# Kernel tuning notes

Measured on AMD Instinct MI355X. Metric: run time of the kernel, lower is better.

## Reference

```python
import jax, jax.numpy as jnp
import numpy as np
from jax import lax

C = 96          # channels (d_model)
D_STATE = 16
D_CONV = 4
EXPAND = 2
D_INNER = EXPAND * C          # 192
DT_RANK = (C + 15) // 16      # 6 (ceil(d_model/16), mamba_ssm default)
B, H, W = 4, 96, 96
LN_EPS = 1e-5


def setup_inputs() -> dict:
    key = jax.random.key(0)
    ks = jax.random.split(key, 10)
    s = 0.02
    return {
        "spatial_feat": jax.random.normal(ks[0], (B, C, H, W), jnp.float32),
        "freq_feat":    jax.random.normal(ks[1], (B, C, H, W), jnp.float32),
        # fusion proj: nn.Linear(2C, C) with bias
        "proj_w": jax.random.normal(ks[2], (C, 2 * C), jnp.float32) * s,
        "proj_b": jnp.zeros((C,), jnp.float32),
        # Mamba params (mamba_ssm defaults: in/x/out proj bias=False, conv bias=True)
        "in_proj_w": jax.random.normal(ks[3], (2 * D_INNER, C), jnp.float32) * s,
        "conv_w": jax.random.normal(ks[4], (D_INNER, 1, D_CONV), jnp.float32) * s,
        "conv_b": jnp.zeros((D_INNER,), jnp.float32),
        "x_proj_w": jax.random.normal(ks[5], (DT_RANK + 2 * D_STATE, D_INNER), jnp.float32) * s,
        "dt_proj_w": jax.random.normal(ks[6], (D_INNER, DT_RANK), jnp.float32) * s,
        "dt_proj_b": jnp.full((D_INNER,), -4.6, jnp.float32),  # softplus ~ 0.01
        "A_log": jnp.log(jnp.tile(jnp.arange(1, D_STATE + 1, dtype=jnp.float32), (D_INNER, 1))),
        "D_param": jnp.ones((D_INNER,), jnp.float32),
        "out_proj_w": jax.random.normal(ks[7], (C, D_INNER), jnp.float32) * s,
        "ln_g": jnp.ones((C,), jnp.float32),
        "ln_b": jnp.zeros((C,), jnp.float32),
    }


def _mamba_fusion(spatial_feat, freq_feat, proj_w, proj_b, in_proj_w, conv_w,
                  conv_b, x_proj_w, dt_proj_w, dt_proj_b, A_log, D_param,
                  out_proj_w, ln_g, ln_b):
    Bsz, Ch, Hh, Ww = spatial_feat.shape
    L = Hh * Ww
    # concat + flatten(2).transpose(1,2): [B, L, 2C]
    seq = jnp.concatenate([spatial_feat, freq_feat], axis=1).reshape(Bsz, 2 * Ch, L).transpose(0, 2, 1)
    x = seq @ proj_w.T + proj_b  # [B, L, C]

    # ---- Mamba mixer ----
    xz = x @ in_proj_w.T                      # [B, L, 2*d_inner]
    x_in, z = jnp.split(xz, 2, axis=-1)
    # causal depthwise conv1d over sequence
    xc = lax.conv_general_dilated(
        x_in.transpose(0, 2, 1), conv_w, (1,), [(D_CONV - 1, 0)],
        dimension_numbers=('NCH', 'OIH', 'NCH'), feature_group_count=D_INNER)
    xc = jax.nn.silu(xc + conv_b[None, :, None]).transpose(0, 2, 1)  # [B, L, d_inner]

    x_dbl = xc @ x_proj_w.T                   # [B, L, dt_rank + 2*d_state]
    dt, Bm, Cm = jnp.split(x_dbl, [DT_RANK, DT_RANK + D_STATE], axis=-1)
    delta = jax.nn.softplus(dt @ dt_proj_w.T + dt_proj_b)  # [B, L, d_inner]
    A = -jnp.exp(A_log)                       # [d_inner, d_state]

    def step(h, inp):
        d_t, B_t, C_t, x_t = inp              # [B,d_in],[B,ds],[B,ds],[B,d_in]
        h = jnp.exp(d_t[:, :, None] * A) * h + (d_t * x_t)[:, :, None] * B_t[:, None, :]
        y_t = jnp.einsum('bds,bs->bd', h, C_t)
        return h, y_t

    xs = (delta.transpose(1, 0, 2), Bm.transpose(1, 0, 2),
          Cm.transpose(1, 0, 2), xc.transpose(1, 0, 2))
    h0 = jnp.zeros((Bsz, D_INNER, D_STATE), x.dtype)
    _, ys = lax.scan(step, h0, xs)            # ys: [L, B, d_inner]
    y = ys.transpose(1, 0, 2) + xc * D_param
    y = y * jax.nn.silu(z)
    mixed = y @ out_proj_w.T                  # [B, L, C]

    # LayerNorm over channel dim
    mu = mixed.mean(-1, keepdims=True)
    var = mixed.var(-1, keepdims=True)
    normed = (mixed - mu) * lax.rsqrt(var + LN_EPS) * ln_g + ln_b

    fused = normed.transpose(0, 2, 1).reshape(Bsz, Ch, Hh, Ww)
    return fused + spatial_feat


def reference(spatial_feat, freq_feat, proj_w, proj_b, in_proj_w, conv_w,
              conv_b, x_proj_w, dt_proj_w, dt_proj_b, A_log, D_param,
              out_proj_w, ln_g, ln_b):
    return _mamba_fusion(spatial_feat, freq_feat, proj_w, proj_b, in_proj_w,
                         conv_w, conv_b, x_proj_w, dt_proj_w, dt_proj_b,
                         A_log, D_param, out_proj_w, ln_g, ln_b)
```

## Files before the change

kernel.cpp:

```cpp
#include <hip/hip_runtime.h>
#include <math.h>

#define kC    96
#define kL    9216
#define kB    4
#define kDI   192
#define kDS   16
#define kDTR  6
#define kCL   128
#define kNC   72
#define kNROW (kB*kL)
#define kNSEQ (kB*kDI*kDS)

__device__ __forceinline__ float silu_f(float v) { return v / (1.f + expf(-v)); }

__global__ __launch_bounds__(256)
void k0_prep(const float* __restrict__ proj_w, const float* __restrict__ proj_b,
             const float* __restrict__ in_proj_w, const float* __restrict__ A_log,
             float* __restrict__ WcT, float* __restrict__ bias_c, float* __restrict__ A)
{
    int idx = blockIdx.x * 256 + threadIdx.x;
    if (idx < 384 * 192) {
        int co = idx / 192;
        int k  = idx % 192;
        float acc = 0.f;
        #pragma unroll 4
        for (int c = 0; c < 96; ++c)
            acc += in_proj_w[co * 96 + c] * proj_w[c * 192 + k];
        WcT[k * 384 + co] = acc;
    }
    if (idx < 384) {
        float acc = 0.f;
        for (int c = 0; c < 96; ++c) acc += in_proj_w[idx * 96 + c] * proj_b[c];
        bias_c[idx] = acc;
    }
    if (idx < kDI * kDS) {
        A[idx] = -expf(A_log[idx]);
    }
}

__global__ __launch_bounds__(256)
void k1_xz(const float* __restrict__ spatial, const float* __restrict__ freq,
           const float* __restrict__ WcT, const float* __restrict__ bias_c,
           float* __restrict__ x_in, float* __restrict__ z)
{
    __shared__ float As[192 * 36];
    const int t   = threadIdx.x;
    const int blk = blockIdx.x;
    const int b   = blk / 288;
    const int l0  = (blk % 288) * 32;

    #pragma unroll
    for (int i = 0; i < 6; ++i) {
        int e  = i * 256 + t;
        int k  = e >> 3, lg = e & 7;
        const float* src = (k < 96)
            ? &spatial[(size_t)(b * 96 + k) * kL]
            : &freq   [(size_t)(b * 96 + (k - 96)) * kL];
        float4 v = *(const float4*)&src[l0 + lg * 4];
        *(float4*)&As[k * 36 + lg * 4] = v;
    }
    __syncthreads();

    const int w    = t >> 6;
    const int lane = t & 63;
    float acc[6][8];
    #pragma unroll
    for (int i = 0; i < 6; ++i) {
        float bc = bias_c[lane + 64 * i];
        #pragma unroll
        for (int l = 0; l < 8; ++l) acc[i][l] = bc;
    }

    const float* wp = WcT + lane;
    #pragma unroll 2
    for (int k = 0; k < 192; ++k) {
        const float4 a0 = *(const float4*)&As[k * 36 + w * 8];
        const float4 a1 = *(const float4*)&As[k * 36 + w * 8 + 4];
        float wv[6];
        #pragma unroll
        for (int i = 0; i < 6; ++i) wv[i] = wp[k * 384 + 64 * i];
        #pragma unroll
        for (int i = 0; i < 6; ++i) {
            acc[i][0] += wv[i] * a0.x;  acc[i][1] += wv[i] * a0.y;
            acc[i][2] += wv[i] * a0.z;  acc[i][3] += wv[i] * a0.w;
            acc[i][4] += wv[i] * a1.x;  acc[i][5] += wv[i] * a1.y;
            acc[i][6] += wv[i] * a1.z;  acc[i][7] += wv[i] * a1.w;
        }
    }

    const size_t rbase = (size_t)b * kL + l0 + w * 8;
    #pragma unroll
    for (int l = 0; l < 8; ++l) {
        const size_t ro = (rbase + l) * 192;
        #pragma unroll
        for (int i = 0; i < 3; ++i)
            x_in[ro + lane + 64 * i] = acc[i][l];
        #pragma unroll
        for (int i = 3; i < 6; ++i)
            z[ro + lane + 64 * i - 192] = acc[i][l];
    }
}

__global__ __launch_bounds__(256)
void k2_conv(const float* __restrict__ x_in, const float* __restrict__ conv_w,
             const float* __restrict__ conv_b, float* __restrict__ xc)
{
    int idx = blockIdx.x * 256 + threadIdx.x;
    if (idx >= kNROW * 48) return;
    const int d4 = idx % 48;
    const int r  = idx / 48;
    const int l  = r % kL;
    const int d0 = d4 * 4;
    float ax = 0.f, ay = 0.f, az = 0.f, aw = 0.f;
    #pragma unroll
    for (int k = 0; k < 4; ++k) {
        int li = l - 3 + k;
        if (li < 0) continue;
        const float4 xv = *(const float4*)&x_in[(size_t)(r - 3 + k) * 192 + d0];
        ax += xv.x * conv_w[(d0 + 0) * 4 + k];
        ay += xv.y * conv_w[(d0 + 1) * 4 + k];
        az += xv.z * conv_w[(d0 + 2) * 4 + k];
        aw += xv.w * conv_w[(d0 + 3) * 4 + k];
    }
    float4 o;
    o.x = silu_f(ax + conv_b[d0 + 0]);
    o.y = silu_f(ay + conv_b[d0 + 1]);
    o.z = silu_f(az + conv_b[d0 + 2]);
    o.w = silu_f(aw + conv_b[d0 + 3]);
    *(float4*)&xc[(size_t)r * 192 + d0] = o;
}

__global__ __launch_bounds__(256)
void k34(const float* __restrict__ xc, const float* __restrict__ x_proj_w,
         const float* __restrict__ dt_proj_w, const float* __restrict__ dt_proj_b,
         float* __restrict__ BC, float* __restrict__ delta)
{
    __shared__ float xcT[192 * 65];
    __shared__ float bc_s[64 * 33];
    __shared__ float dtr_s[64 * 9];
    const int t = threadIdx.x;
    const size_t R0 = (size_t)blockIdx.x * 64;

    #pragma unroll
    for (int i = 0; i < 12; ++i) {
        int e = i * 256 + t;
        int r = e / 48, k4 = e % 48;
        float4 v = *(const float4*)&xc[(R0 + r) * 192 + k4 * 4];
        xcT[(k4 * 4 + 0) * 65 + r] = v.x;
        xcT[(k4 * 4 + 1) * 65 + r] = v.y;
        xcT[(k4 * 4 + 2) * 65 + r] = v.z;
        xcT[(k4 * 4 + 3) * 65 + r] = v.w;
    }
    __syncthreads();

    const int lane = t & 63;
    const int w = __builtin_amdgcn_readfirstlane(t >> 6);

    float acc[10];
    #pragma unroll
    for (int i = 0; i < 10; ++i) acc[i] = 0.f;
    int jj[10];
    #pragma unroll
    for (int i = 0; i < 10; ++i) { int j = w + 4 * i; jj[i] = (j < 38) ? j : 37; }

    #pragma unroll 4
    for (int k = 0; k < 192; ++k) {
        const float xv = xcT[k * 65 + lane];
        #pragma unroll
        for (int i = 0; i < 10; ++i)
            acc[i] += xv * x_proj_w[jj[i] * 192 + k];
    }

    #pragma unroll
    for (int i = 0; i < 10; ++i) {
        int j = w + 4 * i;
        if (j < 6)       dtr_s[lane * 9 + j] = acc[i];
        else if (j < 38) bc_s[lane * 33 + (j - 6)] = acc[i];
    }
    __syncthreads();

    #pragma unroll
    for (int i = 0; i < 2; ++i) {
        int e = i * 256 + t;
        int r = e >> 3, j4 = e & 7;
        float4 v;
        v.x = bc_s[r * 33 + j4 * 4 + 0];
        v.y = bc_s[r * 33 + j4 * 4 + 1];
        v.z = bc_s[r * 33 + j4 * 4 + 2];
        v.w = bc_s[r * 33 + j4 * 4 + 3];
        *(float4*)&BC[(R0 + r) * 32 + j4 * 4] = v;
    }

    {
        float dtv[6];
        #pragma unroll
        for (int j = 0; j < 6; ++j) dtv[j] = dtr_s[lane * 9 + j];
        #pragma unroll 4
        for (int m = 0; m < 48; ++m) {
            const int d = w * 48 + m;
            float a = dt_proj_b[d];
            #pragma unroll
            for (int j = 0; j < 6; ++j) a += dtv[j] * dt_proj_w[d * 6 + j];
            float sp = (a > 20.f) ? a : log1pf(expf(a));
            xcT[d * 65 + lane] = sp;
        }
    }
    __syncthreads();

    #pragma unroll
    for (int i = 0; i < 12; ++i) {
        int e = i * 256 + t;
        int r = e / 48, d4 = e % 48;
        float4 v;
        v.x = xcT[(d4 * 4 + 0) * 65 + r];
        v.y = xcT[(d4 * 4 + 1) * 65 + r];
        v.z = xcT[(d4 * 4 + 2) * 65 + r];
        v.w = xcT[(d4 * 4 + 3) * 65 + r];
        *(float4*)&delta[(R0 + r) * 192 + d4 * 4] = v;
    }
}

__global__ __launch_bounds__(256)
void k5_scan1(const float* __restrict__ delta, const float* __restrict__ xc,
              const float* __restrict__ BC, const float* __restrict__ A,
              float* __restrict__ Pc, float* __restrict__ Sc)
{
    const int wid  = (blockIdx.x * 256 + threadIdx.x) >> 6;
    const int lane = threadIdx.x & 63;
    const int c  = wid % kNC;
    const int dg = (wid / kNC) % 48;
    const int b  = wid / (kNC * 48);
    const int s  = lane & 15;
    const int d  = dg * 4 + (lane >> 4);
    const float Ads = A[dg * 64 + lane];

    const size_t rbase = (size_t)b * kL + (size_t)c * kCL;
    const float* dp = delta + rbase * 192 + d;
    const float* xp = xc    + rbase * 192 + d;
    const float* bp = BC    + rbase * 32  + s;

    float P = 1.f, S = 0.f;
    #pragma unroll 4
    for (int i = 0; i < kCL; ++i) {
        float dv = *dp, xv = *xp, bv = *bp;
        float a  = __expf(dv * Ads);
        float bt = dv * xv * bv;
        P *= a;
        S  = a * S + bt;
        dp += 192; xp += 192; bp += 32;
    }
    const int row = (b * 192 + d) * 16 + s;
    Pc[(size_t)c * kNSEQ + row] = P;
    Sc[(size_t)c * kNSEQ + row] = S;
}

__global__ __launch_bounds__(256)
void k6_cscan(const float* __restrict__ Pc, const float* __restrict__ Sc,
              float* __restrict__ hin)
{
    const int row = blockIdx.x * 256 + threadIdx.x;
    float h = 0.f;
    for (int c = 0; c < kNC; ++c) {
        size_t o = (size_t)c * kNSEQ + row;
        hin[o] = h;
        h = Pc[o] * h + Sc[o];
    }
}

__global__ __launch_bounds__(256)
void k7_scan2(const float* __restrict__ delta, const float* __restrict__ xc,
              const float* __restrict__ BC, const float* __restrict__ A,
              const float* __restrict__ hin, float* __restrict__ ys)
{
    const int wid  = (blockIdx.x * 256 + threadIdx.x) >> 6;
    const int lane = threadIdx.x & 63;
    const int c  = wid % kNC;
    const int dg = (wid / kNC) % 48;
    const int b  = wid / (kNC * 48);
    const int s  = lane & 15;
    const int d  = dg * 4 + (lane >> 4);
    const float Ads = A[dg * 64 + lane];
    const int row = (b * 192 + d) * 16 + s;

    const size_t rbase = (size_t)b * kL + (size_t)c * kCL;
    const float* dp = delta + rbase * 192 + d;
    const float* xp = xc    + rbase * 192 + d;
    const float* bp = BC    + rbase * 32  + s;
    const float* cp = BC    + rbase * 32  + 16 + s;
    float*       yp = ys    + rbase * 192 + d;

    float h = hin[(size_t)c * kNSEQ + row];
    for (int i = 0; i < kCL; ++i) {
        float dv = *dp, xv = *xp, bv = *bp, cv = *cp;
        float a = __expf(dv * Ads);
        h = a * h + dv * xv * bv;
        float pv = h * cv;
        pv += __shfl_xor(pv, 1);
        pv += __shfl_xor(pv, 2);
        pv += __shfl_xor(pv, 4);
        pv += __shfl_xor(pv, 8);
        if (s == 0) *yp = pv;
        dp += 192; xp += 192; bp += 32; cp += 32; yp += 192;
    }
}

__global__ __launch_bounds__(256)
void k8_final(const float* __restrict__ ys, const float* __restrict__ xc,
              const float* __restrict__ z, const float* __restrict__ Dp,
              const float* __restrict__ out_proj_w, const float* __restrict__ ln_g,
              const float* __restrict__ ln_b, const float* __restrict__ spatial,
              float* __restrict__ out)
{
    __shared__ float yt[32 * 196];
    __shared__ float wt[96 * 36];
    const int t = threadIdx.x;
    const size_t r0 = (size_t)blockIdx.x * 32;
    const int b = (int)(r0 / kL);

    #pragma unroll
    for (int i = 0; i < 6; ++i) {
        int e  = i * 256 + t;
        int l  = e / 48, d4 = e % 48;
        size_t r = r0 + l;
        float4 yv = *(const float4*)&ys[r * 192 + d4 * 4];
        float4 xv = *(const float4*)&xc[r * 192 + d4 * 4];
        float4 zv = *(const float4*)&z [r * 192 + d4 * 4];
        float4 Dv = *(const float4*)&Dp[d4 * 4];
        float4 o;
        o.x = (yv.x + xv.x * Dv.x) * silu_f(zv.x);
        o.y = (yv.y + xv.y * Dv.y) * silu_f(zv.y);
        o.z = (yv.z + xv.z * Dv.z) * silu_f(zv.z);
        o.w = (yv.w + xv.w * Dv.w) * silu_f(zv.w);
        *(float4*)&yt[l * 196 + d4 * 4] = o;
    }
    __syncthreads();

    const int l  = t >> 3;
    const int cg = t & 7;
    float acc[12];
    #pragma unroll
    for (int i = 0; i < 12; ++i) acc[i] = 0.f;

    for (int kc = 0; kc < 6; ++kc) {
        __syncthreads();
        #pragma unroll
        for (int i = 0; i < 3; ++i) {
            int e = i * 256 + t;
            int c = e / 8, k4 = e % 8;
            float4 w = *(const float4*)&out_proj_w[c * 192 + kc * 32 + k4 * 4];
            *(float4*)&wt[c * 36 + k4 * 4] = w;
        }
        __syncthreads();
        #pragma unroll
        for (int k4 = 0; k4 < 8; ++k4) {
            float4 yv = *(const float4*)&yt[l * 196 + kc * 32 + k4 * 4];
            #pragma unroll
            for (int i = 0; i < 12; ++i) {
                const float4 wv = *(const float4*)&wt[(cg + 8 * i) * 36 + k4 * 4];
                acc[i] += yv.x * wv.x + yv.y * wv.y + yv.z * wv.z + yv.w * wv.w;
            }
        }
    }

    float sum = 0.f, ss = 0.f;
    #pragma unroll
    for (int i = 0; i < 12; ++i) { sum += acc[i]; ss += acc[i] * acc[i]; }
    #pragma unroll
    for (int m = 1; m < 8; m <<= 1) {
        sum += __shfl_xor(sum, m);
        ss  += __shfl_xor(ss, m);
    }
    const float mu  = sum * (1.f / 96.f);
    const float var = ss * (1.f / 96.f) - mu * mu;
    const float rs  = rsqrtf(var + 1e-5f);
    const int lg = (int)(r0 % kL) + l;
    #pragma unroll
    for (int i = 0; i < 12; ++i) {
        int c = cg + 8 * i;
        float nv = (acc[i] - mu) * rs * ln_g[c] + ln_b[c];
        size_t o = ((size_t)b * 96 + c) * kL + lg;
        out[o] = nv + spatial[o];
    }
}

extern "C" void kernel_launch(void* const* d_in, const int* in_sizes, int n_in,
                              void* d_out, int out_size, void* d_ws, size_t ws_size,
                              hipStream_t stream) {
    const float* spatial    = (const float*)d_in[0];
    const float* freq       = (const float*)d_in[1];
    const float* proj_w     = (const float*)d_in[2];
    const float* proj_b     = (const float*)d_in[3];
    const float* in_proj_w  = (const float*)d_in[4];
    const float* conv_w     = (const float*)d_in[5];
    const float* conv_b     = (const float*)d_in[6];
    const float* x_proj_w   = (const float*)d_in[7];
    const float* dt_proj_w  = (const float*)d_in[8];
    const float* dt_proj_b  = (const float*)d_in[9];
    const float* A_log      = (const float*)d_in[10];
    const float* D_param    = (const float*)d_in[11];
    const float* out_proj_w = (const float*)d_in[12];
    const float* ln_g       = (const float*)d_in[13];
    const float* ln_b       = (const float*)d_in[14];
    float* out = (float*)d_out;

    char* wsb = (char*)d_ws;
    size_t off = 0;
    auto alloc = [&](size_t bytes) -> float* {
        float* p = (float*)(wsb + off);
        off += (bytes + 255) & ~(size_t)255;
        return p;
    };
    float* x_in  = alloc((size_t)kNROW * kDI * 4);
    float* z     = alloc((size_t)kNROW * kDI * 4);
    float* xc    = alloc((size_t)kNROW * kDI * 4);
    float* delta = alloc((size_t)kNROW * kDI * 4);
    float* BC    = alloc((size_t)kNROW * 32 * 4);
    float* Pc    = alloc((size_t)kNC * kNSEQ * 4);
    float* Sc    = alloc((size_t)kNC * kNSEQ * 4);
    float* hin   = alloc((size_t)kNC * kNSEQ * 4);
    float* WcT   = alloc((size_t)192 * 384 * 4);
    float* biasc = alloc(384 * 4);
    float* Aa    = alloc((size_t)kDI * kDS * 4);
    float* ys    = x_in;

    k0_prep <<<288,  256, 0, stream>>>(proj_w, proj_b, in_proj_w, A_log, WcT, biasc, Aa);
    k1_xz   <<<1152, 256, 0, stream>>>(spatial, freq, WcT, biasc, x_in, z);
    k2_conv <<<6912, 256, 0, stream>>>(x_in, conv_w, conv_b, xc);
    k34     <<<576,  256, 0, stream>>>(xc, x_proj_w, dt_proj_w, dt_proj_b, BC, delta);
    k5_scan1<<<3456, 256, 0, stream>>>(delta, xc, BC, Aa, Pc, Sc);
    k6_cscan<<<48,   256, 0, stream>>>(Pc, Sc, hin);
    k7_scan2<<<3456, 256, 0, stream>>>(delta, xc, BC, Aa, hin, ys);
    k8_final<<<1152, 256, 0, stream>>>(ys, xc, z, D_param, out_proj_w, ln_g, ln_b, spatial, out);
}
```

Before: 557.3 us.

## Transpose scan inputs to time-major per channel and precompute delta*x

k34 now writes delta, delta*x and the B/C projections in a channel-major, sequence-contiguous layout. This lets both scan kernels read float4 vectors along time instead of doing strided 192-float loads. The scan2 kernel prefetches the next float4 group and writes its y output in the same transposed layout. k8_final transposes y back through shared memory, which adds LDS work and extra shared memory per block. The transposed stores from k34 are scalar stores that are only partly coalesced.

Result: slower. 608.3 us (+9.1%).

```diff
diff --git a/kernel.cpp b/kernel.cpp
--- a/kernel.cpp
+++ b/kernel.cpp
@@ -134,13 +134,15 @@
 __global__ __launch_bounds__(256)
 void k34(const float* __restrict__ xc, const float* __restrict__ x_proj_w,
          const float* __restrict__ dt_proj_w, const float* __restrict__ dt_proj_b,
-         float* __restrict__ BC, float* __restrict__ delta)
+         float* __restrict__ BCt, float* __restrict__ dT, float* __restrict__ duT)
 {
     __shared__ float xcT[192 * 65];
     __shared__ float bc_s[64 * 33];
     __shared__ float dtr_s[64 * 9];
     const int t = threadIdx.x;
     const size_t R0 = (size_t)blockIdx.x * 64;
+    const int b  = (int)(R0 / kL);
+    const int l0 = (int)(R0 % kL);
 
     #pragma unroll
     for (int i = 0; i < 12; ++i) {
@@ -181,49 +183,30 @@
     __syncthreads();
 
     #pragma unroll
-    for (int i = 0; i < 2; ++i) {
+    for (int i = 0; i < 8; ++i) {
         int e = i * 256 + t;
-        int r = e >> 3, j4 = e & 7;
-        float4 v;
-        v.x = bc_s[r * 33 + j4 * 4 + 0];
-        v.y = bc_s[r * 33 + j4 * 4 + 1];
-        v.z = bc_s[r * 33 + j4 * 4 + 2];
-        v.w = bc_s[r * 33 + j4 * 4 + 3];
-        *(float4*)&BC[(R0 + r) * 32 + j4 * 4] = v;
-    }
-
-    {
-        float dtv[6];
-        #pragma unroll
-        for (int j = 0; j < 6; ++j) dtv[j] = dtr_s[lane * 9 + j];
-        #pragma unroll 4
-        for (int m = 0; m < 48; ++m) {
-            const int d = w * 48 + m;
-            float a = dt_proj_b[d];
-            #pragma unroll
-            for (int j = 0; j < 6; ++j) a += dtv[j] * dt_proj_w[d * 6 + j];
-            float sp = (a > 20.f) ? a : log1pf(expf(a));
-            xcT[d * 65 + lane] = sp;
-        }
-    }
-    __syncthreads();
-
-    #pragma unroll
-    for (int i = 0; i < 12; ++i) {
+        int j = e >> 6, li = e & 63;
+        BCt[((size_t)(b * 32 + j)) * kL + l0 + li] = bc_s[li * 33 + j];
+    }
+
+    #pragma unroll 2
+    for (int i = 0; i < 48; ++i) {
         int e = i * 256 + t;
-        int r = e / 48, d4 = e % 48;
-        float4 v;
-        v.x = xcT[(d4 * 4 + 0) * 65 + r];
-        v.y = xcT[(d4 * 4 + 1) * 65 + r];
-        v.z = xcT[(d4 * 4 + 2) * 65 + r];
-        v.w = xcT[(d4 * 4 + 3) * 65 + r];
-        *(float4*)&delta[(R0 + r) * 192 + d4 * 4] = v;
-    }
-}
-
-__global__ __launch_bounds__(256)
-void k5_scan1(const float* __restrict__ delta, const float* __restrict__ xc,
-              const float* __restrict__ BC, const float* __restrict__ A,
+        int d = e >> 6, li = e & 63;
+        float a = dt_proj_b[d];
+        #pragma unroll
+        for (int j = 0; j < 6; ++j)
+            a += dtr_s[li * 9 + j] * dt_proj_w[d * 6 + j];
+        float sp = (a > 20.f) ? a : log1pf(expf(a));
+        size_t o = ((size_t)(b * 192) + d) * kL + l0 + li;
+        dT[o]  = sp;
+        duT[o] = sp * xcT[d * 65 + li];
+    }
+}
+
+__global__ __launch_bounds__(256)
+void k5_scan1(const float* __restrict__ dT, const float* __restrict__ duT,
+              const float* __restrict__ BCt, const float* __restrict__ A,
               float* __restrict__ Pc, float* __restrict__ Sc)
 {
     const int wid  = (blockIdx.x * 256 + threadIdx.x) >> 6;
@@ -235,20 +218,22 @@
     const int d  = dg * 4 + (lane >> 4);
     const float Ads = A[dg * 64 + lane];
 
-    const size_t rbase = (size_t)b * kL + (size_t)c * kCL;
-    const float* dp = delta + rbase * 192 + d;
-    const float* xp = xc    + rbase * 192 + d;
-    const float* bp = BC    + rbase * 32  + s;
+    const size_t off = ((size_t)(b * 192 + d)) * kL + c * kCL;
+    const float* dp  = dT  + off;
+    const float* dup = duT + off;
+    const float* bp  = BCt + ((size_t)(b * 32 + s)) * kL + c * kCL;
 
     float P = 1.f, S = 0.f;
-    #pragma unroll 4
-    for (int i = 0; i < kCL; ++i) {
-        float dv = *dp, xv = *xp, bv = *bp;
-        float a  = __expf(dv * Ads);
-        float bt = dv * xv * bv;
-        P *= a;
-        S  = a * S + bt;
-        dp += 192; xp += 192; bp += 32;
+    for (int i = 0; i < kCL / 4; ++i) {
+        float4 d4 = *(const float4*)dp;
+        float4 u4 = *(const float4*)dup;
+        float4 b4 = *(const float4*)bp;
+        dp += 4; dup += 4; bp += 4;
+        float a;
+        a = __expf(d4.x * Ads); P *= a; S = a * S + u4.x * b4.x;
+        a = __expf(d4.y * Ads); P *= a; S = a * S + u4.y * b4.y;
+        a = __expf(d4.z * Ads); P *= a; S = a * S + u4.z * b4.z;
+        a = __expf(d4.w * Ads); P *= a; S = a * S + u4.w * b4.w;
     }
     const int row = (b * 192 + d) * 16 + s;
     Pc[(size_t)c * kNSEQ + row] = P;
@@ -269,9 +254,9 @@
 }
 
 __global__ __launch_bounds__(256)
-void k7_scan2(const float* __restrict__ delta, const float* __restrict__ xc,
-              const float* __restrict__ BC, const float* __restrict__ A,
-              const float* __restrict__ hin, float* __restrict__ ys)
+void k7_scan2(const float* dT, const float* __restrict__ duT,
+              const float* __restrict__ BCt, const float* __restrict__ A,
+              const float* __restrict__ hin, float* yT)
 {
     const int wid  = (blockIdx.x * 256 + threadIdx.x) >> 6;
     const int lane = threadIdx.x & 63;
@@ -283,58 +268,96 @@
     const float Ads = A[dg * 64 + lane];
     const int row = (b * 192 + d) * 16 + s;
 
-    const size_t rbase = (size_t)b * kL + (size_t)c * kCL;
-    const float* dp = delta + rbase * 192 + d;
-    const float* xp = xc    + rbase * 192 + d;
-    const float* bp = BC    + rbase * 32  + s;
-    const float* cp = BC    + rbase * 32  + 16 + s;
-    float*       yp = ys    + rbase * 192 + d;
+    const size_t off = ((size_t)(b * 192 + d)) * kL + c * kCL;
+    const float* dp  = dT  + off;
+    const float* dup = duT + off;
+    const float* bp  = BCt + ((size_t)(b * 32 + s)) * kL + c * kCL;
+    const float* cp  = bp + (size_t)16 * kL;
+    float*       yp  = yT + off;
 
     float h = hin[(size_t)c * kNSEQ + row];
-    for (int i = 0; i < kCL; ++i) {
-        float dv = *dp, xv = *xp, bv = *bp, cv = *cp;
-        float a = __expf(dv * Ads);
-        h = a * h + dv * xv * bv;
-        float pv = h * cv;
-        pv += __shfl_xor(pv, 1);
-        pv += __shfl_xor(pv, 2);
-        pv += __shfl_xor(pv, 4);
-        pv += __shfl_xor(pv, 8);
-        if (s == 0) *yp = pv;
-        dp += 192; xp += 192; bp += 32; cp += 32; yp += 192;
-    }
-}
-
-__global__ __launch_bounds__(256)
-void k8_final(const float* __restrict__ ys, const float* __restrict__ xc,
+
+    float4 d4 = *(const float4*)dp;   dp  += 4;
+    float4 u4 = *(const float4*)dup;  dup += 4;
+    float4 b4 = *(const float4*)bp;   bp  += 4;
+    float4 c4 = *(const float4*)cp;   cp  += 4;
+
+    for (int i = 0; i < kCL / 4; ++i) {
+        float4 nd = d4, nu = u4, nb = b4, nc = c4;
+        if (i + 1 < kCL / 4) {
+            nd = *(const float4*)dp;   dp  += 4;
+            nu = *(const float4*)dup;  dup += 4;
+            nb = *(const float4*)bp;   bp  += 4;
+            nc = *(const float4*)cp;   cp  += 4;
+        }
+        float4 y4;
+        float a, pv;
+        a = __expf(d4.x * Ads); h = a * h + u4.x * b4.x; pv = h * c4.x;
+        pv += __shfl_xor(pv, 1); pv += __shfl_xor(pv, 2);
+        pv += __shfl_xor(pv, 4); pv += __shfl_xor(pv, 8);
+        y4.x = pv;
+        a = __expf(d4.y * Ads); h = a * h + u4.y * b4.y; pv = h * c4.y;
+        pv += __shfl_xor(pv, 1); pv += __shfl_xor(pv, 2);
+        pv += __shfl_xor(pv, 4); pv += __shfl_xor(pv, 8);
+        y4.y = pv;
+        a = __expf(d4.z * Ads); h = a * h + u4.z * b4.z; pv = h * c4.z;
+        pv += __shfl_xor(pv, 1); pv += __shfl_xor(pv, 2);
+        pv += __shfl_xor(pv, 4); pv += __shfl_xor(pv, 8);
+        y4.z = pv;
+        a = __expf(d4.w * Ads); h = a * h + u4.w * b4.w; pv = h * c4.w;
+        pv += __shfl_xor(pv, 1); pv += __shfl_xor(pv, 2);
+        pv += __shfl_xor(pv, 4); pv += __shfl_xor(pv, 8);
+        y4.w = pv;
+
+        if (s == 0) *(float4*)yp = y4;
+        yp += 4;
+        d4 = nd; u4 = nu; b4 = nb; c4 = nc;
+    }
+}
+
+__global__ __launch_bounds__(256)
+void k8_final(const float* __restrict__ yT, const float* __restrict__ xc,
               const float* __restrict__ z, const float* __restrict__ Dp,
               const float* __restrict__ out_proj_w, const float* __restrict__ ln_g,
               const float* __restrict__ ln_b, const float* __restrict__ spatial,
               float* __restrict__ out)
 {
     __shared__ float yt[32 * 196];
+    __shared__ float ps[32 * 196];
     __shared__ float wt[96 * 36];
     const int t = threadIdx.x;
     const size_t r0 = (size_t)blockIdx.x * 32;
-    const int b = (int)(r0 / kL);
+    const int b  = (int)(r0 / kL);
+    const int l0 = (int)(r0 % kL);
 
     #pragma unroll
     for (int i = 0; i < 6; ++i) {
         int e  = i * 256 + t;
         int l  = e / 48, d4 = e % 48;
         size_t r = r0 + l;
-        float4 yv = *(const float4*)&ys[r * 192 + d4 * 4];
         float4 xv = *(const float4*)&xc[r * 192 + d4 * 4];
         float4 zv = *(const float4*)&z [r * 192 + d4 * 4];
         float4 Dv = *(const float4*)&Dp[d4 * 4];
-        float4 o;
-        o.x = (yv.x + xv.x * Dv.x) * silu_f(zv.x);
-        o.y = (yv.y + xv.y * Dv.y) * silu_f(zv.y);
-        o.z = (yv.z + xv.z * Dv.z) * silu_f(zv.z);
-        o.w = (yv.w + xv.w * Dv.w) * silu_f(zv.w);
-        *(float4*)&yt[l * 196 + d4 * 4] = o;
+        float4 p, q;
+        p.x = silu_f(zv.x); q.x = xv.x * Dv.x * p.x;
+        p.y = silu_f(zv.y); q.y = xv.y * Dv.y * p.y;
+        p.z = silu_f(zv.z); q.z = xv.z * Dv.z * p.z;
+        p.w = silu_f(zv.w); q.w = xv.w * Dv.w * p.w;
+        *(float4*)&yt[l * 196 + d4 * 4] = q;
+        *(float4*)&ps[l * 196 + d4 * 4] = p;
     }
     __syncthreads();
+
+    #pragma unroll
+    for (int i = 0; i < 6; ++i) {
+        int e  = i * 256 + t;
+        int dd = e >> 3, lf = e & 7;
+        float4 yv = *(const float4*)&yT[((size_t)(b * 192) + dd) * kL + l0 + lf * 4];
+        yt[(lf * 4 + 0) * 196 + dd] += yv.x * ps[(lf * 4 + 0) * 196 + dd];
+        yt[(lf * 4 + 1) * 196 + dd] += yv.y * ps[(lf * 4 + 1) * 196 + dd];
+        yt[(lf * 4 + 2) * 196 + dd] += yv.z * ps[(lf * 4 + 2) * 196 + dd];
+        yt[(lf * 4 + 3) * 196 + dd] += yv.w * ps[(lf * 4 + 3) * 196 + dd];
+    }
 
     const int l  = t >> 3;
     const int cg = t & 7;
@@ -374,7 +397,7 @@
     const float mu  = sum * (1.f / 96.f);
     const float var = ss * (1.f / 96.f) - mu * mu;
     const float rs  = rsqrtf(var + 1e-5f);
-    const int lg = (int)(r0 % kL) + l;
+    const int lg = l0 + l;
     #pragma unroll
     for (int i = 0; i < 12; ++i) {
         int c = cg + 8 * i;
@@ -414,22 +437,23 @@
     float* x_in  = alloc((size_t)kNROW * kDI * 4);
     float* z     = alloc((size_t)kNROW * kDI * 4);
     float* xc    = alloc((size_t)kNROW * kDI * 4);
-    float* delta = alloc((size_t)kNROW * kDI * 4);
-    float* BC    = alloc((size_t)kNROW * 32 * 4);
+    float* dT    = alloc((size_t)kNROW * kDI * 4);
+    float* BCt   = alloc((size_t)kB * 32 * kL * 4);
     float* Pc    = alloc((size_t)kNC * kNSEQ * 4);
     float* Sc    = alloc((size_t)kNC * kNSEQ * 4);
     float* hin   = alloc((size_t)kNC * kNSEQ * 4);
     float* WcT   = alloc((size_t)192 * 384 * 4);
     float* biasc = alloc(384 * 4);
     float* Aa    = alloc((size_t)kDI * kDS * 4);
-    float* ys    = x_in;
+    float* duT   = x_in;
+    float* yT    = dT;
 
     k0_prep <<<288,  256, 0, stream>>>(proj_w, proj_b, in_proj_w, A_log, WcT, biasc, Aa);
     k1_xz   <<<1152, 256, 0, stream>>>(spatial, freq, WcT, biasc, x_in, z);
     k2_conv <<<6912, 256, 0, stream>>>(x_in, conv_w, conv_b, xc);
-    k34     <<<576,  256, 0, stream>>>(xc, x_proj_w, dt_proj_w, dt_proj_b, BC, delta);
-    k5_scan1<<<3456, 256, 0, stream>>>(delta, xc, BC, Aa, Pc, Sc);
+    k34     <<<576,  256, 0, stream>>>(xc, x_proj_w, dt_proj_w, dt_proj_b, BCt, dT, duT);
+    k5_scan1<<<3456, 256, 0, stream>>>(dT, duT, BCt, Aa, Pc, Sc);
     k6_cscan<<<48,   256, 0, stream>>>(Pc, Sc, hin);
-    k7_scan2<<<3456, 256, 0, stream>>>(delta, xc, BC, Aa, hin, ys);
-    k8_final<<<1152, 256, 0, stream>>>(ys, xc, z, D_param, out_proj_w, ln_g, ln_b, spatial, out);
-}
+    k7_scan2<<<3456, 256, 0, stream>>>(dT, duT, BCt, Aa, hin, yT);
+    k8_final<<<1152, 256, 0, stream>>>(yT, xc, z, D_param, out_proj_w, ln_g, ln_b, spatial, out);
+}
```
